# Optimization experiments

Hardware: AMD Instinct MI355X
Metric: run time of the kernel (lower is better)

The kernel has to match this reference:

```python
import jax, jax.numpy as jnp
import numpy as np

B, T, D = 4, 4096, 1024
HD = 64              # head_dim
H = D // HD          # n_heads = 16
C = 64               # chunk_size (T % C == 0)


def setup_inputs() -> dict:
    key = jax.random.key(0)
    k1, k2, k3 = jax.random.split(key, 3)
    out = jax.random.normal(k1, (B, T, D), jnp.float32)
    # Linear(d_model, d_model, bias=False) weights, ~1/sqrt(D) scale
    W_write = jax.random.normal(k2, (D, D), jnp.float32) * 0.03
    W_read = jax.random.normal(k3, (D, D), jnp.float32) * 0.03
    decay = jnp.full((H,), 4.6, jnp.float32)                 # torch init value
    log_alpha = jnp.log(jnp.full((H,), 0.03, jnp.float32))   # memory_alpha=0.03
    return {"out": out, "W_write": W_write, "W_read": W_read,
            "decay": decay, "log_alpha": log_alpha}


def reference(out, W_write, W_read, decay, log_alpha):
    Bb, Tt, Dd = out.shape
    d, Hh, Cc = HD, D // HD, C
    out32 = out.astype(jnp.float32)
    gamma = jax.nn.sigmoid(decay)          # (H,)
    log_gamma = jnp.log(gamma)

    # projections and head split: (B, H, T, d)
    v = (out32 @ W_write.T).reshape(Bb, Tt, Hh, d).transpose(0, 2, 1, 3)
    rk = out32.reshape(Bb, Tt, Hh, d).transpose(0, 2, 1, 3)
    wk = jnp.pad(rk[:, :, :-1], ((0, 0), (0, 0), (1, 0), (0, 0)))  # shift right by 1

    BH = Bb * Hh
    gamma_bh = jnp.tile(gamma, Bb)          # (BH,) index b*H+h -> gamma[h]
    log_gamma_bh = jnp.tile(log_gamma, Bb)
    nC = Tt // Cc
    # (nC, BH, C, d) so lax.scan runs over chunks
    v_ch = v.reshape(BH, nC, Cc, d).transpose(1, 0, 2, 3)
    rk_ch = rk.reshape(BH, nC, Cc, d).transpose(1, 0, 2, 3)
    wk_ch = wk.reshape(BH, nC, Cc, d).transpose(1, 0, 2, 3)

    p = jnp.arange(Cc)
    diffs = jnp.clip(p[:, None] - 1 - p[None, :], 0)          # (C, C)
    causal = p[:, None] > p[None, :]
    # per-(b,h) intra-chunk decay mask (BH, C, C)
    M = jnp.exp(diffs[None].astype(jnp.float32) * log_gamma_bh[:, None, None]) * causal[None]
    g_p = gamma_bh[:, None] ** p[None, :].astype(jnp.float32)            # (BH, C)
    g_w = gamma_bh[:, None] ** (Cc - 1 - p)[None, :].astype(jnp.float32)  # (BH, C)
    g_C = gamma_bh ** Cc                                                  # (BH,)

    def scan_fn(W, chunk):
        rk_c, wk_c, v_c = chunk                                   # each (BH, C, d)
        inter = jnp.einsum('bij,bcj->bci', W, rk_c) * g_p[:, :, None]
        S = jnp.einsum('bcd,bkd->bck', rk_c, wk_c)                # (BH, C, C)
        intra = jnp.einsum('bck,bkd->bcd', S * M, v_c)
        W_new = g_C[:, None, None] * W + jnp.einsum('bci,bcj->bij', v_c * g_w[:, :, None], wk_c)
        return W_new, inter + intra

    W0 = jnp.zeros((BH, d, d), jnp.float32)
    _, reads = jax.lax.scan(scan_fn, W0, (rk_ch, wk_ch, v_ch))   # (nC, BH, C, d)
    reads = reads.transpose(1, 0, 2, 3).reshape(Bb, Hh, Tt, d)
    alpha = jnp.exp(log_alpha)[None, :, None, None]
    reads = (alpha * reads).transpose(0, 2, 1, 3).reshape(Bb, Tt, Dd)
    return out + (reads @ W_read.T).astype(out.dtype)
```

## Files before the change

### kernel.cpp

```cpp
#include <hip/hip_runtime.h>
#include <hip/hip_bf16.h>
#include <stdint.h>


typedef __bf16 bf16x8 __attribute__((ext_vector_type(8)));
typedef float f32x4 __attribute__((ext_vector_type(4)));

#define GAS __attribute__((address_space(1)))
#define LAS __attribute__((address_space(3)))

__device__ __forceinline__ unsigned short f2bf(float f) {
  unsigned u = __float_as_uint(f);
  u = (u + 0x7fffu + ((u >> 16) & 1u)) >> 16;
  return (unsigned short)u;
}
__device__ __forceinline__ float bf2f(unsigned short h) {
  return __uint_as_float(((unsigned)h) << 16);
}

__global__ __launch_bounds__(256) void cast_f32_to_bf16(
    const float* __restrict__ src, unsigned short* __restrict__ dst, int n8) {
  int i = blockIdx.x * 256 + threadIdx.x;
  if (i >= n8) return;
  const float4* s = (const float4*)src + (size_t)i * 2;
  float4 f0 = s[0], f1 = s[1];
  union { uint4 u4; unsigned short us[8]; } o;
  o.us[0] = f2bf(f0.x); o.us[1] = f2bf(f0.y); o.us[2] = f2bf(f0.z); o.us[3] = f2bf(f0.w);
  o.us[4] = f2bf(f1.x); o.us[5] = f2bf(f1.y); o.us[6] = f2bf(f1.z); o.us[7] = f2bf(f1.w);
  ((uint4*)dst)[i] = o.u4;
}

__global__ __launch_bounds__(256) void cast_weights(
    const float* __restrict__ w1, const float* __restrict__ w2,
    unsigned short* __restrict__ dst) {
  int i = blockIdx.x * 256 + threadIdx.x;
  const float* src = (i < 131072) ? w1 : w2;
  int j = (i < 131072) ? i : i - 131072;
  const float4* s = (const float4*)src + (size_t)j * 2;
  float4 f0 = s[0], f1 = s[1];
  union { uint4 u4; unsigned short us[8]; } o;
  o.us[0] = f2bf(f0.x); o.us[1] = f2bf(f0.y); o.us[2] = f2bf(f0.z); o.us[3] = f2bf(f0.w);
  o.us[4] = f2bf(f1.x); o.us[5] = f2bf(f1.y); o.us[6] = f2bf(f1.z); o.us[7] = f2bf(f1.w);
  ((uint4*)dst)[i] = o.u4;
}

__device__ __forceinline__ void swizzle_bm_bn(int id, int& bm, int& bn) {
  int x = id & 7;
  int s = id >> 3;
  bn = s & 7;
  bm = ((s >> 3) << 3) | x;
}

__global__ __launch_bounds__(256, 4) void gemm_bt_bf16out(
    const unsigned short* __restrict__ A, const unsigned short* __restrict__ B,
    unsigned short* __restrict__ C, int M, int N, int K) {
  __shared__ unsigned short As[2][128 * 32];
  __shared__ unsigned short Bs[2][128 * 32];
  int tid = threadIdx.x;
  int l = tid & 63, w = tid >> 6;
  int bm, bn;
  swizzle_bm_bn(blockIdx.x, bm, bn);
  int wm = (w >> 1) * 64, wn = (w & 1) * 64;
  f32x4 acc[4][4];
#pragma unroll
  for (int mi = 0; mi < 4; mi++)
#pragma unroll
    for (int ni = 0; ni < 4; ni++) acc[mi][ni] = (f32x4){0.f, 0.f, 0.f, 0.f};
  const unsigned short* Ab = A + (size_t)bm * 128 * K;
  const unsigned short* Bb = B + (size_t)bn * 128 * K;
  int lr = l >> 2, lc = (l & 3) * 8;
  int lm = l & 15, q4 = l >> 4;
  const int nit = K >> 5;
#pragma unroll
  for (int q = 0; q < 2; q++) {
    int g = (w * 2 + q) * 16 + lr;
    __builtin_amdgcn_global_load_lds((GAS void*)(void*)(Ab + (size_t)g * K + lc),
                                     (LAS void*)(&As[0][(w * 2 + q) * 512]), 16, 0, 0);
    __builtin_amdgcn_global_load_lds((GAS void*)(void*)(Bb + (size_t)g * K + lc),
                                     (LAS void*)(&Bs[0][(w * 2 + q) * 512]), 16, 0, 0);
  }
  for (int it = 0; it < nit; it++) {
    __syncthreads();
    int buf = it & 1;
    if (it + 1 < nit) {
      int k0 = (it + 1) << 5;
#pragma unroll
      for (int q = 0; q < 2; q++) {
        int g = (w * 2 + q) * 16 + lr;
        __builtin_amdgcn_global_load_lds((GAS void*)(void*)(Ab + (size_t)g * K + k0 + lc),
                                         (LAS void*)(&As[buf ^ 1][(w * 2 + q) * 512]), 16, 0, 0);
        __builtin_amdgcn_global_load_lds((GAS void*)(void*)(Bb + (size_t)g * K + k0 + lc),
                                         (LAS void*)(&Bs[buf ^ 1][(w * 2 + q) * 512]), 16, 0, 0);
      }
    }
    bf16x8 a[4], b[4];
#pragma unroll
    for (int mi = 0; mi < 4; mi++) a[mi] = *(const bf16x8*)&As[buf][(wm + mi * 16 + lm) * 32 + q4 * 8];
#pragma unroll
    for (int ni = 0; ni < 4; ni++) b[ni] = *(const bf16x8*)&Bs[buf][(wn + ni * 16 + lm) * 32 + q4 * 8];
#pragma unroll
    for (int mi = 0; mi < 4; mi++)
#pragma unroll
      for (int ni = 0; ni < 4; ni++)
        acc[mi][ni] = __builtin_amdgcn_mfma_f32_16x16x32_bf16(a[mi], b[ni], acc[mi][ni], 0, 0, 0);
  }
#pragma unroll
  for (int mi = 0; mi < 4; mi++)
#pragma unroll
    for (int ni = 0; ni < 4; ni++) {
      int r0 = bm * 128 + wm + mi * 16 + q4 * 4;
      int col = bn * 128 + wn + ni * 16 + lm;
#pragma unroll
      for (int j = 0; j < 4; j++)
        C[(size_t)(r0 + j) * N + col] = f2bf(acc[mi][ni][j]);
    }
}

__global__ __launch_bounds__(256, 4) void gemm_bt_addout(
    const unsigned short* __restrict__ A, const unsigned short* __restrict__ B,
    const unsigned short* __restrict__ base_bf, float* __restrict__ C, int M, int N, int K) {
  __shared__ unsigned short As[2][128 * 32];
  __shared__ unsigned short Bs[2][128 * 32];
  int tid = threadIdx.x;
  int l = tid & 63, w = tid >> 6;
  int bm, bn;
  swizzle_bm_bn(blockIdx.x, bm, bn);
  int wm = (w >> 1) * 64, wn = (w & 1) * 64;
  int lr = l >> 2, lc = (l & 3) * 8;
  int lm = l & 15, q4 = l >> 4;
  f32x4 acc[4][4];
#pragma unroll
  for (int mi = 0; mi < 4; mi++)
#pragma unroll
    for (int ni = 0; ni < 4; ni++) {
      int r0 = bm * 128 + wm + mi * 16 + q4 * 4;
      int col = bn * 128 + wn + ni * 16 + lm;
#pragma unroll
      for (int j = 0; j < 4; j++)
        acc[mi][ni][j] = bf2f(base_bf[(size_t)(r0 + j) * N + col]);
    }
  const unsigned short* Ab = A + (size_t)bm * 128 * K;
  const unsigned short* Bb = B + (size_t)bn * 128 * K;
  const int nit = K >> 5;
#pragma unroll
  for (int q = 0; q < 2; q++) {
    int g = (w * 2 + q) * 16 + lr;
    __builtin_amdgcn_global_load_lds((GAS void*)(void*)(Ab + (size_t)g * K + lc),
                                     (LAS void*)(&As[0][(w * 2 + q) * 512]), 16, 0, 0);
    __builtin_amdgcn_global_load_lds((GAS void*)(void*)(Bb + (size_t)g * K + lc),
                                     (LAS void*)(&Bs[0][(w * 2 + q) * 512]), 16, 0, 0);
  }
  for (int it = 0; it < nit; it++) {
    __syncthreads();
    int buf = it & 1;
    if (it + 1 < nit) {
      int k0 = (it + 1) << 5;
#pragma unroll
      for (int q = 0; q < 2; q++) {
        int g = (w * 2 + q) * 16 + lr;
        __builtin_amdgcn_global_load_lds((GAS void*)(void*)(Ab + (size_t)g * K + k0 + lc),
                                         (LAS void*)(&As[buf ^ 1][(w * 2 + q) * 512]), 16, 0, 0);
        __builtin_amdgcn_global_load_lds((GAS void*)(void*)(Bb + (size_t)g * K + k0 + lc),
                                         (LAS void*)(&Bs[buf ^ 1][(w * 2 + q) * 512]), 16, 0, 0);
      }
    }
    bf16x8 a[4], b[4];
#pragma unroll
    for (int mi = 0; mi < 4; mi++) a[mi] = *(const bf16x8*)&As[buf][(wm + mi * 16 + lm) * 32 + q4 * 8];
#pragma unroll
    for (int ni = 0; ni < 4; ni++) b[ni] = *(const bf16x8*)&Bs[buf][(wn + ni * 16 + lm) * 32 + q4 * 8];
#pragma unroll
    for (int mi = 0; mi < 4; mi++)
#pragma unroll
      for (int ni = 0; ni < 4; ni++)
        acc[mi][ni] = __builtin_amdgcn_mfma_f32_16x16x32_bf16(a[mi], b[ni], acc[mi][ni], 0, 0, 0);
  }
#pragma unroll
  for (int mi = 0; mi < 4; mi++)
#pragma unroll
    for (int ni = 0; ni < 4; ni++) {
      int r0 = bm * 128 + wm + mi * 16 + q4 * 4;
      int col = bn * 128 + wn + ni * 16 + lm;
#pragma unroll
      for (int j = 0; j < 4; j++)
        C[(size_t)(r0 + j) * N + col] = acc[mi][ni][j];
    }
}

__global__ __launch_bounds__(256) void chunk_local(
    const unsigned short* __restrict__ rkg,
    const unsigned short* __restrict__ vg,
    const float* __restrict__ decay,
    unsigned short* __restrict__ intra_bf,
    unsigned short* __restrict__ U_bf) {
  int c = blockIdx.x, bh = blockIdx.y;
  int b = bh >> 4, h = bh & 15;
  int tid = threadIdx.x, l = tid & 63, w = tid >> 6;
  float gamma = 1.0f / (1.0f + __expf(-decay[h]));
  float lg = __logf(gamma);

  __shared__ unsigned short rk_s[64 * 72];
  __shared__ unsigned short wk_s[64 * 72];
  __shared__ unsigned short wkT_s[64 * 72];
  __shared__ unsigned short vT_s[64 * 72];
  __shared__ unsigned short S_s[64 * 72];

  const size_t rowbase = (((size_t)b * 4096 + (size_t)c * 64) * 1024) + h * 64;

#pragma unroll
  for (int r = 0; r < 2; r++) {
    int e = r * 256 + tid;
    int p = e >> 3, seg = e & 7;
    uint4 dr = *(const uint4*)(rkg + rowbase + (size_t)p * 1024 + seg * 8);
    *(uint4*)&rk_s[p * 72 + seg * 8] = dr;
    uint4 dv = *(const uint4*)(vg + rowbase + (size_t)p * 1024 + seg * 8);
    {
      unsigned uu[4] = {dv.x, dv.y, dv.z, dv.w};
#pragma unroll
      for (int qq = 0; qq < 4; qq++) {
        vT_s[(seg * 8 + qq * 2) * 72 + p] = (unsigned short)(uu[qq] & 0xffffu);
        vT_s[(seg * 8 + qq * 2 + 1) * 72 + p] = (unsigned short)(uu[qq] >> 16);
      }
    }
    int tg = c * 64 + p - 1;
    uint4 dw = make_uint4(0u, 0u, 0u, 0u);
    if (tg >= 0) dw = *(const uint4*)(rkg + ((size_t)b * 4096 + tg) * 1024 + h * 64 + seg * 8);
    *(uint4*)&wk_s[p * 72 + seg * 8] = dw;
    {
      unsigned uu[4] = {dw.x, dw.y, dw.z, dw.w};
#pragma unroll
      for (int qq = 0; qq < 4; qq++) {
        wkT_s[(seg * 8 + qq * 2) * 72 + p] = (unsigned short)(uu[qq] & 0xffffu);
        wkT_s[(seg * 8 + qq * 2 + 1) * 72 + p] = (unsigned short)(uu[qq] >> 16);
      }
    }
  }
  __syncthreads();

  int lm = l & 15, q4 = l >> 4;

  {
    bf16x8 a0 = *(const bf16x8*)&rk_s[(w * 16 + lm) * 72 + q4 * 8];
    bf16x8 a1 = *(const bf16x8*)&rk_s[(w * 16 + lm) * 72 + 32 + q4 * 8];
#pragma unroll
    for (int ni = 0; ni < 4; ni++) {
      bf16x8 b0 = *(const bf16x8*)&wk_s[(ni * 16 + lm) * 72 + q4 * 8];
      bf16x8 b1 = *(const bf16x8*)&wk_s[(ni * 16 + lm) * 72 + 32 + q4 * 8];
      f32x4 acc = {0.f, 0.f, 0.f, 0.f};
      acc = __builtin_amdgcn_mfma_f32_16x16x32_bf16(a0, b0, acc, 0, 0, 0);
      acc = __builtin_amdgcn_mfma_f32_16x16x32_bf16(a1, b1, acc, 0, 0, 0);
#pragma unroll
      for (int j = 0; j < 4; j++) {
        int p = w * 16 + q4 * 4 + j;
        int q = ni * 16 + lm;
        float m = (p > q) ? __expf(lg * (float)(p - 1 - q)) : 0.0f;
        S_s[p * 72 + q] = f2bf(acc[j] * m);
      }
    }
  }
  __syncthreads();

  {
    bf16x8 a0 = *(const bf16x8*)&S_s[(w * 16 + lm) * 72 + q4 * 8];
    bf16x8 a1 = *(const bf16x8*)&S_s[(w * 16 + lm) * 72 + 32 + q4 * 8];
#pragma unroll
    for (int ni = 0; ni < 4; ni++) {
      bf16x8 b0 = *(const bf16x8*)&vT_s[(ni * 16 + lm) * 72 + q4 * 8];
      bf16x8 b1 = *(const bf16x8*)&vT_s[(ni * 16 + lm) * 72 + 32 + q4 * 8];
      f32x4 acc = {0.f, 0.f, 0.f, 0.f};
      acc = __builtin_amdgcn_mfma_f32_16x16x32_bf16(a0, b0, acc, 0, 0, 0);
      acc = __builtin_amdgcn_mfma_f32_16x16x32_bf16(a1, b1, acc, 0, 0, 0);
#pragma unroll
      for (int j = 0; j < 4; j++) {
        int p = w * 16 + q4 * 4 + j;
        int i = ni * 16 + lm;
        intra_bf[rowbase + (size_t)p * 1024 + i] = f2bf(acc[j]);
      }
    }
  }

  {
    bf16x8 a0 = *(const bf16x8*)&vT_s[(w * 16 + lm) * 72 + q4 * 8];
    bf16x8 a1 = *(const bf16x8*)&vT_s[(w * 16 + lm) * 72 + 32 + q4 * 8];
#pragma unroll
    for (int jj = 0; jj < 8; jj++) {
      int p0 = q4 * 8 + jj;
      a0[jj] = (__bf16)((float)a0[jj] * __expf(lg * (float)(63 - p0)));
      a1[jj] = (__bf16)((float)a1[jj] * __expf(lg * (float)(63 - (p0 + 32))));
    }
    size_t ub = ((size_t)bh * 64 + c) * 4096;
#pragma unroll
    for (int nj = 0; nj < 4; nj++) {
      bf16x8 b0 = *(const bf16x8*)&wkT_s[(nj * 16 + lm) * 72 + q4 * 8];
      bf16x8 b1 = *(const bf16x8*)&wkT_s[(nj * 16 + lm) * 72 + 32 + q4 * 8];
      f32x4 acc = {0.f, 0.f, 0.f, 0.f};
      acc = __builtin_amdgcn_mfma_f32_16x16x32_bf16(a0, b0, acc, 0, 0, 0);
      acc = __builtin_amdgcn_mfma_f32_16x16x32_bf16(a1, b1, acc, 0, 0, 0);
#pragma unroll
      for (int j = 0; j < 4; j++) {
        int i = w * 16 + q4 * 4 + j;
        int col = nj * 16 + lm;
        U_bf[ub + i * 64 + col] = f2bf(acc[j]);
      }
    }
  }
}

__global__ __launch_bounds__(256) void scan_w(
    const unsigned short* __restrict__ U_bf, const float* __restrict__ decay,
    unsigned short* __restrict__ Wst) {
  int nsl = blockIdx.x, bh = blockIdx.y;
  int h = bh & 15;
  float gamma = 1.0f / (1.0f + __expf(-decay[h]));
  float gC = __expf(64.0f * __logf(gamma));
  int n0 = nsl * 512 + threadIdx.x * 2;
  const unsigned short* Ub = U_bf + (size_t)bh * 64 * 4096 + n0;
  unsigned short* Wb = Wst + (size_t)bh * 64 * 4096 + n0;
  float w0 = 0.f, w1 = 0.f;
#pragma unroll
  for (int c = 0; c < 64; c++) {
    unsigned u = *(const unsigned*)(Ub + (size_t)c * 4096);
    ushort2 sv;
    sv.x = f2bf(w0);
    sv.y = f2bf(w1);
    *(ushort2*)(Wb + (size_t)c * 4096) = sv;
    w0 = gC * w0 + bf2f((unsigned short)(u & 0xffffu));
    w1 = gC * w1 + bf2f((unsigned short)(u >> 16));
  }
}

__global__ __launch_bounds__(256) void inter_combine(
    const unsigned short* __restrict__ rkg, const unsigned short* __restrict__ Wst,
    const unsigned short* __restrict__ intra_bf,
    const float* __restrict__ decay, const float* __restrict__ log_alpha,
    unsigned short* __restrict__ reads_bf) {
  int c = blockIdx.x, bh = blockIdx.y;
  int b = bh >> 4, h = bh & 15;
  int tid = threadIdx.x, l = tid & 63, w = tid >> 6;
  int lm = l & 15, q4 = l >> 4;
  float gamma = 1.0f / (1.0f + __expf(-decay[h]));
  float lg = __logf(gamma);
  float alpha = __expf(log_alpha[h]);

  __shared__ unsigned short rk_s[64 * 72];
  __shared__ unsigned short W_s[64 * 72];
  __shared__ unsigned short in_s[64 * 72];

  const size_t rowbase = (((size_t)b * 4096 + (size_t)c * 64) * 1024) + h * 64;
  const size_t wbase = ((size_t)bh * 64 + c) * 4096;

#pragma unroll
  for (int r = 0; r < 2; r++) {
    int e = r * 256 + tid;
    int p = e >> 3, seg = (e & 7) * 8;
    *(uint4*)&rk_s[p * 72 + seg] = *(const uint4*)(rkg + rowbase + (size_t)p * 1024 + seg);
    *(uint4*)&in_s[p * 72 + seg] = *(const uint4*)(intra_bf + rowbase + (size_t)p * 1024 + seg);
    *(uint4*)&W_s[p * 72 + seg] = *(const uint4*)(Wst + wbase + (size_t)p * 64 + seg);
  }
  __syncthreads();

  bf16x8 a0 = *(const bf16x8*)&rk_s[(w * 16 + lm) * 72 + q4 * 8];
  bf16x8 a1 = *(const bf16x8*)&rk_s[(w * 16 + lm) * 72 + 32 + q4 * 8];
#pragma unroll
  for (int ni = 0; ni < 4; ni++) {
    bf16x8 b0 = *(const bf16x8*)&W_s[(ni * 16 + lm) * 72 + q4 * 8];
    bf16x8 b1 = *(const bf16x8*)&W_s[(ni * 16 + lm) * 72 + 32 + q4 * 8];
    f32x4 acc = {0.f, 0.f, 0.f, 0.f};
    acc = __builtin_amdgcn_mfma_f32_16x16x32_bf16(a0, b0, acc, 0, 0, 0);
    acc = __builtin_amdgcn_mfma_f32_16x16x32_bf16(a1, b1, acc, 0, 0, 0);
#pragma unroll
    for (int j = 0; j < 4; j++) {
      int p = w * 16 + q4 * 4 + j;
      int i = ni * 16 + lm;
      float gp = __expf(lg * (float)p);
      reads_bf[rowbase + (size_t)p * 1024 + i] =
          f2bf(alpha * (acc[j] * gp + bf2f(in_s[p * 72 + i])));
    }
  }
}

extern "C" void kernel_launch(void* const* d_in, const int* in_sizes, int n_in,
                              void* d_out, int out_size, void* d_ws, size_t ws_size,
                              hipStream_t stream) {
  const float* out_f = (const float*)d_in[0];
  const float* Ww = (const float*)d_in[1];
  const float* Wr = (const float*)d_in[2];
  const float* decay = (const float*)d_in[3];
  const float* lalpha = (const float*)d_in[4];

  char* ws = (char*)d_ws;
  unsigned short* outbf = (unsigned short*)(ws + 0);
  unsigned short* vbf   = (unsigned short*)(ws + 33554432);
  unsigned short* wwbf  = (unsigned short*)(ws + 67108864);
  unsigned short* wrbf  = (unsigned short*)(ws + 69206016);
  unsigned short* intra = (unsigned short*)(ws + 71303168);
  unsigned short* U     = (unsigned short*)(ws + 104857600);
  unsigned short* Wst   = (unsigned short*)(ws + 138412032);
  unsigned short* reads = (unsigned short*)(ws + 171966464);

  cast_f32_to_bf16<<<dim3(8192), 256, 0, stream>>>(out_f, outbf, 16777216 / 8);
  cast_weights<<<dim3(1024), 256, 0, stream>>>(Ww, Wr, wwbf);

  gemm_bt_bf16out<<<dim3(1024), 256, 0, stream>>>(outbf, wwbf, vbf, 16384, 1024, 1024);

  chunk_local<<<dim3(64, 64), 256, 0, stream>>>(outbf, vbf, decay, intra, U);

  scan_w<<<dim3(8, 64), 256, 0, stream>>>(U, decay, Wst);
  inter_combine<<<dim3(64, 64), 256, 0, stream>>>(outbf, Wst, intra, decay, lalpha, reads);

  gemm_bt_addout<<<dim3(1024), 256, 0, stream>>>(reads, wrbf, outbf, (float*)d_out,
                                                 16384, 1024, 1024);
}
```

Measured before the change: 288.0 us.

## Deepen GEMM LDS pipeline to four stages with explicit vmcnt waits

Both projection GEMMs switch from a double-buffered LDS pipeline to a four-buffer ring that prefetches three K-tiles ahead. Explicit s_waitcnt vmcnt counts wait only for the tile about to be consumed, and raw s_barrier calls replace __syncthreads so later loads stay in flight. In the add-out GEMM, the prologue loads are also issued before the residual base values are read, so the two overlap. LDS per block doubles to 64KB, which can cut occupancy below the requested 4 blocks per CU, and the hand-set vmcnt values depend on each stage issuing exactly four loads.

```diff
diff --git a/kernel.cpp b/kernel.cpp
--- a/kernel.cpp
+++ b/kernel.cpp
@@ -51,11 +51,20 @@
   bm = ((s >> 3) << 3) | x;
 }
 
+#define STAGE4(Adst, Bdst, kofs)                                                            \
+  _Pragma("unroll") for (int q = 0; q < 2; q++) {                                           \
+    int g = (w * 2 + q) * 16 + lr;                                                          \
+    __builtin_amdgcn_global_load_lds((GAS void*)(void*)(Ab + (size_t)g * K + (kofs) + lc),  \
+                                     (LAS void*)((Adst) + (w * 2 + q) * 512), 16, 0, 0);    \
+    __builtin_amdgcn_global_load_lds((GAS void*)(void*)(Bb + (size_t)g * K + (kofs) + lc),  \
+                                     (LAS void*)((Bdst) + (w * 2 + q) * 512), 16, 0, 0);    \
+  }
+
 __global__ __launch_bounds__(256, 4) void gemm_bt_bf16out(
     const unsigned short* __restrict__ A, const unsigned short* __restrict__ B,
     unsigned short* __restrict__ C, int M, int N, int K) {
-  __shared__ unsigned short As[2][128 * 32];
-  __shared__ unsigned short Bs[2][128 * 32];
+  __shared__ unsigned short As[4][128 * 32];
+  __shared__ unsigned short Bs[4][128 * 32];
   int tid = threadIdx.x;
   int l = tid & 63, w = tid >> 6;
   int bm, bn;
@@ -72,27 +81,21 @@
   int lm = l & 15, q4 = l >> 4;
   const int nit = K >> 5;
 #pragma unroll
-  for (int q = 0; q < 2; q++) {
-    int g = (w * 2 + q) * 16 + lr;
-    __builtin_amdgcn_global_load_lds((GAS void*)(void*)(Ab + (size_t)g * K + lc),
-                                     (LAS void*)(&As[0][(w * 2 + q) * 512]), 16, 0, 0);
-    __builtin_amdgcn_global_load_lds((GAS void*)(void*)(Bb + (size_t)g * K + lc),
-                                     (LAS void*)(&Bs[0][(w * 2 + q) * 512]), 16, 0, 0);
-  }
+  for (int t = 0; t < 3; t++) STAGE4(&As[t][0], &Bs[t][0], t << 5)
   for (int it = 0; it < nit; it++) {
-    __syncthreads();
-    int buf = it & 1;
-    if (it + 1 < nit) {
-      int k0 = (it + 1) << 5;
-#pragma unroll
-      for (int q = 0; q < 2; q++) {
-        int g = (w * 2 + q) * 16 + lr;
-        __builtin_amdgcn_global_load_lds((GAS void*)(void*)(Ab + (size_t)g * K + k0 + lc),
-                                         (LAS void*)(&As[buf ^ 1][(w * 2 + q) * 512]), 16, 0, 0);
-        __builtin_amdgcn_global_load_lds((GAS void*)(void*)(Bb + (size_t)g * K + k0 + lc),
-                                         (LAS void*)(&Bs[buf ^ 1][(w * 2 + q) * 512]), 16, 0, 0);
-      }
-    }
+    __builtin_amdgcn_s_barrier();
+    if (it + 3 < nit) {
+      int t = it + 3;
+      STAGE4(&As[t & 3][0], &Bs[t & 3][0], t << 5)
+    }
+    int rem = nit - 1 - it;
+    if (rem >= 3)      asm volatile("s_waitcnt vmcnt(12)" ::: "memory");
+    else if (rem == 2) asm volatile("s_waitcnt vmcnt(8)" ::: "memory");
+    else if (rem == 1) asm volatile("s_waitcnt vmcnt(4)" ::: "memory");
+    else               asm volatile("s_waitcnt vmcnt(0)" ::: "memory");
+    __builtin_amdgcn_s_barrier();
+    __builtin_amdgcn_sched_barrier(0);
+    int buf = it & 3;
     bf16x8 a[4], b[4];
 #pragma unroll
     for (int mi = 0; mi < 4; mi++) a[mi] = *(const bf16x8*)&As[buf][(wm + mi * 16 + lm) * 32 + q4 * 8];
@@ -119,8 +122,8 @@
 __global__ __launch_bounds__(256, 4) void gemm_bt_addout(
     const unsigned short* __restrict__ A, const unsigned short* __restrict__ B,
     const unsigned short* __restrict__ base_bf, float* __restrict__ C, int M, int N, int K) {
-  __shared__ unsigned short As[2][128 * 32];
-  __shared__ unsigned short Bs[2][128 * 32];
+  __shared__ unsigned short As[4][128 * 32];
+  __shared__ unsigned short Bs[4][128 * 32];
   int tid = threadIdx.x;
   int l = tid & 63, w = tid >> 6;
   int bm, bn;
@@ -128,6 +131,11 @@
   int wm = (w >> 1) * 64, wn = (w & 1) * 64;
   int lr = l >> 2, lc = (l & 3) * 8;
   int lm = l & 15, q4 = l >> 4;
+  const unsigned short* Ab = A + (size_t)bm * 128 * K;
+  const unsigned short* Bb = B + (size_t)bn * 128 * K;
+  const int nit = K >> 5;
+#pragma unroll
+  for (int t = 0; t < 3; t++) STAGE4(&As[t][0], &Bs[t][0], t << 5)
   f32x4 acc[4][4];
 #pragma unroll
   for (int mi = 0; mi < 4; mi++)
@@ -139,31 +147,20 @@
       for (int j = 0; j < 4; j++)
         acc[mi][ni][j] = bf2f(base_bf[(size_t)(r0 + j) * N + col]);
     }
-  const unsigned short* Ab = A + (size_t)bm * 128 * K;
-  const unsigned short* Bb = B + (size_t)bn * 128 * K;
-  const int nit = K >> 5;
-#pragma unroll
-  for (int q = 0; q < 2; q++) {
-    int g = (w * 2 + q) * 16 + lr;
-    __builtin_amdgcn_global_load_lds((GAS void*)(void*)(Ab + (size_t)g * K + lc),
-                                     (LAS void*)(&As[0][(w * 2 + q) * 512]), 16, 0, 0);
-    __builtin_amdgcn_global_load_lds((GAS void*)(void*)(Bb + (size_t)g * K + lc),
-                                     (LAS void*)(&Bs[0][(w * 2 + q) * 512]), 16, 0, 0);
-  }
   for (int it = 0; it < nit; it++) {
-    __syncthreads();
-    int buf = it & 1;
-    if (it + 1 < nit) {
-      int k0 = (it + 1) << 5;
-#pragma unroll
-      for (int q = 0; q < 2; q++) {
-        int g = (w * 2 + q) * 16 + lr;
-        __builtin_amdgcn_global_load_lds((GAS void*)(void*)(Ab + (size_t)g * K + k0 + lc),
-                                         (LAS void*)(&As[buf ^ 1][(w * 2 + q) * 512]), 16, 0, 0);
-        __builtin_amdgcn_global_load_lds((GAS void*)(void*)(Bb + (size_t)g * K + k0 + lc),
-                                         (LAS void*)(&Bs[buf ^ 1][(w * 2 + q) * 512]), 16, 0, 0);
-      }
-    }
+    __builtin_amdgcn_s_barrier();
+    if (it + 3 < nit) {
+      int t = it + 3;
+      STAGE4(&As[t & 3][0], &Bs[t & 3][0], t << 5)
+    }
+    int rem = nit - 1 - it;
+    if (rem >= 3)      asm volatile("s_waitcnt vmcnt(12)" ::: "memory");
+    else if (rem == 2) asm volatile("s_waitcnt vmcnt(8)" ::: "memory");
+    else if (rem == 1) asm volatile("s_waitcnt vmcnt(4)" ::: "memory");
+    else               asm volatile("s_waitcnt vmcnt(0)" ::: "memory");
+    __builtin_amdgcn_s_barrier();
+    __builtin_amdgcn_sched_barrier(0);
+    int buf = it & 3;
     bf16x8 a[4], b[4];
 #pragma unroll
     for (int mi = 0; mi < 4; mi++) a[mi] = *(const bf16x8*)&As[buf][(wm + mi * 16 + lm) * 32 + q4 * 8];
```

After: 303.6 us. 1.05x slower.
